# Kernel tuning notes

Hardware: AMD Instinct MI355X
Metric: run time of the kernel (lower is better)

The kernel has to match this reference:

```python
import jax, jax.numpy as jnp
import numpy as np

BASE_THETA = 0.5
K_DOP = 0.2
K_NOR = 0.15
K_SERO = 0.1
DIM = 1024


def setup_inputs() -> dict:
    key = jax.random.key(0)
    ks = jax.random.split(key, 9)
    scale = 1.0 / np.sqrt(DIM)
    x = jax.random.normal(ks[0], (2, 2048, DIM), dtype=jnp.float32)
    Wq = jax.random.normal(ks[1], (DIM, DIM), dtype=jnp.float32) * scale
    bq = jnp.zeros((DIM,), dtype=jnp.float32)
    Wk = jax.random.normal(ks[2], (DIM, DIM), dtype=jnp.float32) * scale
    bk = jnp.zeros((DIM,), dtype=jnp.float32)
    Wv = jax.random.normal(ks[3], (DIM, DIM), dtype=jnp.float32) * scale
    bv = jnp.zeros((DIM,), dtype=jnp.float32)
    Wo = jax.random.normal(ks[4], (DIM, DIM), dtype=jnp.float32) * scale
    bo = jnp.zeros((DIM,), dtype=jnp.float32)
    return {"x": x, "Wq": Wq, "bq": bq, "Wk": Wk, "bk": bk,
            "Wv": Wv, "bv": bv, "Wo": Wo, "bo": bo}


def reference(x, Wq, bq, Wk, bk, Wv, bv, Wo, bo):
    # Projections: torch nn.Linear computes x @ W.T + b
    q = jnp.einsum('bsd,ed->bse', x, Wq) + bq
    k = jnp.einsum('bsd,ed->bse', x, Wk) + bk
    v = jnp.einsum('bsd,ed->bse', x, Wv) + bv
    # Full [B, S, S] scores (no 1/sqrt(d) scaling in the original)
    qk = jnp.einsum('bsd,btd->bst', q, k)
    theta = (BASE_THETA
             + K_DOP * jax.nn.sigmoid(qk)
             + K_NOR * jnp.tanh(qk)
             + K_SERO * jax.nn.relu(qk))
    attn = jax.nn.softmax(theta, axis=-1)
    out = jnp.einsum('bst,btd->bsd', attn, v)
    return jnp.einsum('bsd,ed->bse', out, Wo) + bo
```

## Files before the change

kernel.cpp:

```cpp
#include <hip/hip_runtime.h>
#include <hip/hip_fp16.h>
#include <stdint.h>

typedef _Float16 f16;
typedef __attribute__((ext_vector_type(8))) _Float16 f16x8;
typedef __attribute__((ext_vector_type(4))) _Float16 f16x4;
typedef __attribute__((ext_vector_type(4))) float f32x4;

#define SEQ 2048
#define DIM 1024
#define NBATCH 2
#define MTOT 4096

__global__ void fill_kernel(float* p, float v, int n){
  int i = blockIdx.x * 256 + threadIdx.x;
  if (i < n) p[i] = v;
}

__global__ void cvt_all(const float* __restrict__ x, const float* __restrict__ Wq,
                        const float* __restrict__ Wk, const float* __restrict__ Wv,
                        const float* __restrict__ Wo,
                        f16* __restrict__ x16, f16* __restrict__ Wcat, f16* __restrict__ Wo16,
                        float* __restrict__ rowacc){
  int b = blockIdx.x;
  if (b == 8192){
    float4 z = {0.f, 0.f, 0.f, 0.f};
#pragma unroll
    for (int i = 0; i < 4; i++) ((float4*)rowacc)[threadIdx.x + i * 256] = z;
    return;
  }
  const float* src; f16* dst; int i;
  if (b < 4096){
    src = x; dst = x16; i = b * 256 + threadIdx.x;
  } else {
    int t = (b - 4096) >> 10;
    i = ((b - 4096) & 1023) * 256 + threadIdx.x;
    src = t == 0 ? Wq : t == 1 ? Wk : t == 2 ? Wv : Wo;
    dst = (t == 3) ? Wo16 : Wcat + (size_t)t * DIM * DIM;
  }
  float4 v = ((const float4*)src)[i];
  ((f16x4*)dst)[i] = (f16x4){(f16)v.x, (f16)v.y, (f16)v.z, (f16)v.w};
}

#define GLOAD16(SRC, DST) __builtin_amdgcn_global_load_lds( \
    (__attribute__((address_space(1))) void*)(SRC), \
    (__attribute__((address_space(3))) void*)(DST), 16, 0, 0)

template<int MODE>
__global__ __launch_bounds__(256, 2)
void gemm_k64(const f16* __restrict__ A, const f16* __restrict__ B,
              int K, int lda, int ldb, long bsA, long bsB, long bsC,
              float* __restrict__ Cf, f16* __restrict__ Ch, f16* __restrict__ vT,
              const float* __restrict__ bias0, const float* __restrict__ bias1,
              const float* __restrict__ bias2, float* __restrict__ rowacc,
              int ldc)
{
  __shared__ __align__(16) f16 As[8192];
  __shared__ __align__(16) f16 Bs[8192];
  const int tid  = threadIdx.x;
  const int lane = tid & 63;
  const int wid  = tid >> 6;
  const int bm = blockIdx.x, bn = blockIdx.y, bz = blockIdx.z;

  const int s_r  = tid >> 3;
  const int s_cb = (tid & 7) ^ (s_r & 7);
  const f16* Abase = A + (long)bz * bsA + (long)(bm * 128 + s_r) * lda + s_cb * 8;
  const f16* Bbase = B + (long)bz * bsB + (long)(bn * 128 + s_r) * ldb + s_cb * 8;

#define STG(T) do{ \
    GLOAD16(Abase + (long)(T)*64,                  &As[       tid*8]); \
    GLOAD16(Abase + (long)(T)*64 + (long)32 * lda, &As[2048 + tid*8]); \
    GLOAD16(Abase + (long)(T)*64 + (long)64 * lda, &As[4096 + tid*8]); \
    GLOAD16(Abase + (long)(T)*64 + (long)96 * lda, &As[6144 + tid*8]); \
    GLOAD16(Bbase + (long)(T)*64,                  &Bs[       tid*8]); \
    GLOAD16(Bbase + (long)(T)*64 + (long)32 * ldb, &Bs[2048 + tid*8]); \
    GLOAD16(Bbase + (long)(T)*64 + (long)64 * ldb, &Bs[4096 + tid*8]); \
    GLOAD16(Bbase + (long)(T)*64 + (long)96 * ldb, &Bs[6144 + tid*8]); \
  }while(0)

  const int l15 = lane & 15, l7 = lane & 7, lhi = lane >> 4;
  const int wrow = (wid >> 1) * 64;
  const int wcol = (wid & 1) * 64;
  const int ar = (wrow + l15) * 64;
  const int br = (wcol + l15) * 64;
  const int cb0 = ((0 + lhi) ^ l7) * 8;
  const int cb1 = ((4 + lhi) ^ l7) * 8;

  f32x4 acc[4][4] = {};
  const int NT = K >> 6;

  for (int t = 0; t < NT; ++t){
    __syncthreads();
    STG(t);
    __syncthreads();
    f16x8 af[4], bf[4];
#pragma unroll
    for (int i = 0; i < 4; i++) af[i] = *(const f16x8*)&As[ar + i * 1024 + cb0];
#pragma unroll
    for (int j = 0; j < 4; j++) bf[j] = *(const f16x8*)&Bs[br + j * 1024 + cb0];
#pragma unroll
    for (int i = 0; i < 4; i++)
#pragma unroll
      for (int j = 0; j < 4; j++)
        acc[i][j] = __builtin_amdgcn_mfma_f32_16x16x32_f16(af[i], bf[j], acc[i][j], 0, 0, 0);
#pragma unroll
    for (int i = 0; i < 4; i++) af[i] = *(const f16x8*)&As[ar + i * 1024 + cb1];
#pragma unroll
    for (int j = 0; j < 4; j++) bf[j] = *(const f16x8*)&Bs[br + j * 1024 + cb1];
#pragma unroll
    for (int i = 0; i < 4; i++)
#pragma unroll
      for (int j = 0; j < 4; j++)
        acc[i][j] = __builtin_amdgcn_mfma_f32_16x16x32_f16(af[i], bf[j], acc[i][j], 0, 0, 0);
  }
#undef STG

  const int cc = l15;
  const int rr = lhi * 4;

  if constexpr (MODE == 0){
#pragma unroll
    for (int i = 0; i < 4; i++)
#pragma unroll
      for (int j = 0; j < 4; j++){
        const int col = bn * 128 + wcol + j * 16 + cc;
        const float badd = bias0 ? bias0[col] : 0.f;
#pragma unroll
        for (int r = 0; r < 4; r++){
          const int row = bm * 128 + wrow + i * 16 + rr + r;
          Cf[(long)bz * bsC + (long)row * ldc + col] = acc[i][j][r] + badd;
        }
      }
  } else if constexpr (MODE == 2){
#pragma unroll
    for (int i = 0; i < 4; i++)
#pragma unroll
      for (int r = 0; r < 4; r++){
        const int row = bm * 128 + wrow + i * 16 + rr + r;
        const float inv = 1.f / rowacc[bz * SEQ + row];
#pragma unroll
        for (int j = 0; j < 4; j++){
          const int col = bn * 128 + wcol + j * 16 + cc;
          Ch[(long)bz * bsC + (long)row * ldc + col] = (f16)(acc[i][j][r] * inv);
        }
      }
  } else if constexpr (MODE == 4){
#pragma unroll
    for (int i = 0; i < 4; i++)
#pragma unroll
      for (int j = 0; j < 4; j++){
        const int col = bn * 128 + wcol + j * 16 + cc;
        if (col < 2048){
          const float badd = (col < 1024) ? bias0[col] : bias1[col - 1024];
#pragma unroll
          for (int r = 0; r < 4; r++){
            const int row = bm * 128 + wrow + i * 16 + rr + r;
            Ch[(long)row * ldc + col] = (f16)(acc[i][j][r] + badd);
          }
        } else {
          const int d = col - 2048;
          const float badd = bias2[d];
          const int row0 = bm * 128 + wrow + i * 16 + rr;
          const int b2 = row0 >> 11, t0 = row0 & 2047;
          f16x4 pk = {(f16)(acc[i][j][0] + badd), (f16)(acc[i][j][1] + badd),
                      (f16)(acc[i][j][2] + badd), (f16)(acc[i][j][3] + badd)};
          *(f16x4*)&vT[(long)b2 * DIM * SEQ + (long)d * SEQ + t0] = pk;
        }
      }
  } else {
#pragma unroll
    for (int i = 0; i < 4; i++)
#pragma unroll
      for (int r = 0; r < 4; r++){
        const int row = bm * 128 + wrow + i * 16 + rr + r;
        float rs = 0.f;
#pragma unroll
        for (int j = 0; j < 4; j++){
          const int col = bn * 128 + wcol + j * 16 + cc;
          const float v = acc[i][j][r];
          const float e1 = __expf(-v);
          const float sg = 1.f / (1.f + e1);
          const float e2 = e1 * e1;
          const float th = 2.f / (1.f + e2) - 1.f;
          const float theta = 0.5f + 0.2f * sg + 0.15f * th + 0.1f * fmaxf(v, 0.f);
          const float P = __expf(fminf(theta - 10.f, 11.f));
          Ch[(long)bz * bsC + (long)row * ldc + col] = (f16)P;
          rs += P;
        }
        rs += __shfl_xor(rs, 1, 64);
        rs += __shfl_xor(rs, 2, 64);
        rs += __shfl_xor(rs, 4, 64);
        rs += __shfl_xor(rs, 8, 64);
        if (cc == 0) atomicAdd(&rowacc[bz * SEQ + row], rs);
      }
  }
}

extern "C" void kernel_launch(void* const* d_in, const int* in_sizes, int n_in,
                              void* d_out, int out_size, void* d_ws, size_t ws_size,
                              hipStream_t stream){
  const float* x  = (const float*)d_in[0];
  const float* Wq = (const float*)d_in[1];
  const float* bq = (const float*)d_in[2];
  const float* Wk = (const float*)d_in[3];
  const float* bk = (const float*)d_in[4];
  const float* Wv = (const float*)d_in[5];
  const float* bv = (const float*)d_in[6];
  const float* Wo = (const float*)d_in[7];
  const float* bo = (const float*)d_in[8];
  float* out = (float*)d_out;

  char* ws = (char*)d_ws;
  size_t off = 0;
  auto alloc = [&](size_t bytes) -> char* {
    char* p = ws + off; off += (bytes + 255) & ~(size_t)255; return p;
  };

  f16* x16     = (f16*)alloc(2ull * MTOT * DIM);
  f16* Wcat    = (f16*)alloc(2ull * 3 * DIM * DIM);
  f16* Wo16    = (f16*)alloc(2ull * DIM * DIM);
  f16* qkcat   = (f16*)alloc(2ull * MTOT * 2 * DIM);
  f16* vT      = (f16*)alloc(2ull * NBATCH * DIM * SEQ);
  f16* Pbuf    = (f16*)alloc(2ull * NBATCH * SEQ * SEQ);
  f16* outb    = (f16*)alloc(2ull * MTOT * DIM);
  float* rowac = (float*)alloc(4ull * MTOT);

  if (off > ws_size){
    fill_kernel<<<(out_size + 255) / 256, 256, 0, stream>>>(out, 12345.0f, out_size);
    return;
  }

  cvt_all<<<8193, 256, 0, stream>>>(x, Wq, Wk, Wv, Wo, x16, Wcat, Wo16, rowac);

  gemm_k64<4><<<dim3(MTOT / 128, 3 * DIM / 128, 1), 256, 0, stream>>>(
      x16, Wcat, DIM, DIM, DIM, 0, 0, 0,
      nullptr, qkcat, vT, bq, bk, bv, nullptr, 2 * DIM);

  gemm_k64<5><<<dim3(SEQ / 128, SEQ / 128, NBATCH), 256, 0, stream>>>(
      qkcat, qkcat + DIM, DIM, 2 * DIM, 2 * DIM,
      (long)SEQ * 2 * DIM, (long)SEQ * 2 * DIM, (long)SEQ * SEQ,
      nullptr, Pbuf, nullptr, nullptr, nullptr, nullptr, rowac, SEQ);

  gemm_k64<2><<<dim3(SEQ / 128, DIM / 128, NBATCH), 256, 0, stream>>>(
      Pbuf, vT, SEQ, SEQ, SEQ,
      (long)SEQ * SEQ, (long)DIM * SEQ, (long)SEQ * DIM,
      nullptr, outb, nullptr, nullptr, nullptr, nullptr, rowac, DIM);

  gemm_k64<0><<<dim3(MTOT / 128, DIM / 128, 1), 256, 0, stream>>>(
      outb, Wo16, DIM, DIM, DIM, 0, 0, 0,
      out, nullptr, nullptr, bo, nullptr, nullptr, nullptr, DIM);
}
```

Baseline: 139.2 us.

## Reassociate output projection into V and triple-buffer GEMM LDS pipeline

Computes V·Wo^T before attention, so P·(V Wo^T) plus normalization and bias produces the output directly and the separate output-projection pass over the attention result is dropped. The new V·Wo GEMM writes its result transposed for the PV GEMM. All GEMMs also switch from a K=64 single-buffer loop with two barriers per step to a K=32 three-stage LDS ring that uses async global-to-LDS loads, vmcnt waits and one barrier per step, with occupancy raised to 3 blocks per CU. The reassociation keeps the FLOP count the same, since the extra GEMM matches the one removed. The main gain is expected from overlapping loads with compute, at the cost of more rounding because V Wo is stored as f16.

Result: slower. 146.8 us (+5.5%).

```diff
diff --git a/kernel.cpp b/kernel.cpp
--- a/kernel.cpp
+++ b/kernel.cpp
@@ -47,102 +47,92 @@
     (__attribute__((address_space(3))) void*)(DST), 16, 0, 0)
 
 template<int MODE>
-__global__ __launch_bounds__(256, 2)
-void gemm_k64(const f16* __restrict__ A, const f16* __restrict__ B,
-              int K, int lda, int ldb, long bsA, long bsB, long bsC,
-              float* __restrict__ Cf, f16* __restrict__ Ch, f16* __restrict__ vT,
-              const float* __restrict__ bias0, const float* __restrict__ bias1,
-              const float* __restrict__ bias2, float* __restrict__ rowacc,
-              int ldc)
+__global__ __launch_bounds__(256, 3)
+void gemm_p3(const f16* __restrict__ A, const f16* __restrict__ B,
+             int K, int lda, int ldb, long bsA, long bsB, long bsC,
+             float* __restrict__ Cf, f16* __restrict__ Ch, f16* __restrict__ Ct,
+             const float* __restrict__ bias0, const float* __restrict__ bias1,
+             const float* __restrict__ bias2, float* __restrict__ rowacc,
+             int ldc)
 {
-  __shared__ __align__(16) f16 As[8192];
-  __shared__ __align__(16) f16 Bs[8192];
+  __shared__ __align__(16) f16 As[3][4096];
+  __shared__ __align__(16) f16 Bs[3][4096];
   const int tid  = threadIdx.x;
   const int lane = tid & 63;
   const int wid  = tid >> 6;
   const int bm = blockIdx.x, bn = blockIdx.y, bz = blockIdx.z;
 
-  const int s_r  = tid >> 3;
-  const int s_cb = (tid & 7) ^ (s_r & 7);
-  const f16* Abase = A + (long)bz * bsA + (long)(bm * 128 + s_r) * lda + s_cb * 8;
-  const f16* Bbase = B + (long)bz * bsB + (long)(bn * 128 + s_r) * ldb + s_cb * 8;
-
-#define STG(T) do{ \
-    GLOAD16(Abase + (long)(T)*64,                  &As[       tid*8]); \
-    GLOAD16(Abase + (long)(T)*64 + (long)32 * lda, &As[2048 + tid*8]); \
-    GLOAD16(Abase + (long)(T)*64 + (long)64 * lda, &As[4096 + tid*8]); \
-    GLOAD16(Abase + (long)(T)*64 + (long)96 * lda, &As[6144 + tid*8]); \
-    GLOAD16(Bbase + (long)(T)*64,                  &Bs[       tid*8]); \
-    GLOAD16(Bbase + (long)(T)*64 + (long)32 * ldb, &Bs[2048 + tid*8]); \
-    GLOAD16(Bbase + (long)(T)*64 + (long)64 * ldb, &Bs[4096 + tid*8]); \
-    GLOAD16(Bbase + (long)(T)*64 + (long)96 * ldb, &Bs[6144 + tid*8]); \
+  long aoff[2], boff[2];
+#pragma unroll
+  for (int l = 0; l < 2; l++){
+    const int r64 = (l * 256 + tid) >> 3;
+    const int cb  = (tid & 7) ^ (r64 & 7);
+    const int grow = r64 + 64 * (cb >> 2);
+    const int gk   = (cb & 3) * 8;
+    aoff[l] = (long)(bm * 128 + grow) * lda + gk;
+    boff[l] = (long)(bn * 128 + grow) * ldb + gk;
+  }
+  const f16* Ag = A + (long)bz * bsA;
+  const f16* Bg = B + (long)bz * bsB;
+
+#define STG(E, T) do{ \
+    GLOAD16(Ag + aoff[0] + (long)(T)*32, &As[E][       tid*8]); \
+    GLOAD16(Ag + aoff[1] + (long)(T)*32, &As[E][2048 + tid*8]); \
+    GLOAD16(Bg + boff[0] + (long)(T)*32, &Bs[E][       tid*8]); \
+    GLOAD16(Bg + boff[1] + (long)(T)*32, &Bs[E][2048 + tid*8]); \
   }while(0)
 
-  const int l15 = lane & 15, l7 = lane & 7, lhi = lane >> 4;
+  const int l15 = lane & 15, lhi = lane >> 4;
   const int wrow = (wid >> 1) * 64;
   const int wcol = (wid & 1) * 64;
-  const int ar = (wrow + l15) * 64;
-  const int br = (wcol + l15) * 64;
-  const int cb0 = ((0 + lhi) ^ l7) * 8;
-  const int cb1 = ((4 + lhi) ^ l7) * 8;
+  const int rga = wrow >> 6, rgb = wcol >> 6;
+  int aadr[4], badr[4];
+#pragma unroll
+  for (int i = 0; i < 4; i++){
+    aadr[i] = (i * 16 + l15) * 64 + (((rga * 4 + lhi) ^ (l15 & 7)) * 8);
+    badr[i] = (i * 16 + l15) * 64 + (((rgb * 4 + lhi) ^ (l15 & 7)) * 8);
+  }
 
   f32x4 acc[4][4] = {};
-  const int NT = K >> 6;
+  const int NT = K >> 5;
+
+  STG(0, 0);
+  STG(1, 1);
+  int d = 0, e = 2;
 
   for (int t = 0; t < NT; ++t){
-    __syncthreads();
-    STG(t);
-    __syncthreads();
+    if (t + 1 < NT) asm volatile("s_waitcnt vmcnt(4)" ::: "memory");
+    else            asm volatile("s_waitcnt vmcnt(0)" ::: "memory");
+    __builtin_amdgcn_s_barrier();
+    if (t + 2 < NT) STG(e, t + 2);
     f16x8 af[4], bf[4];
 #pragma unroll
-    for (int i = 0; i < 4; i++) af[i] = *(const f16x8*)&As[ar + i * 1024 + cb0];
-#pragma unroll
-    for (int j = 0; j < 4; j++) bf[j] = *(const f16x8*)&Bs[br + j * 1024 + cb0];
+    for (int i = 0; i < 4; i++) af[i] = *(const f16x8*)&As[d][aadr[i]];
+#pragma unroll
+    for (int j = 0; j < 4; j++) bf[j] = *(const f16x8*)&Bs[d][badr[j]];
 #pragma unroll
     for (int i = 0; i < 4; i++)
 #pragma unroll
       for (int j = 0; j < 4; j++)
         acc[i][j] = __builtin_amdgcn_mfma_f32_16x16x32_f16(af[i], bf[j], acc[i][j], 0, 0, 0);
-#pragma unroll
-    for (int i = 0; i < 4; i++) af[i] = *(const f16x8*)&As[ar + i * 1024 + cb1];
-#pragma unroll
-    for (int j = 0; j < 4; j++) bf[j] = *(const f16x8*)&Bs[br + j * 1024 + cb1];
-#pragma unroll
-    for (int i = 0; i < 4; i++)
-#pragma unroll
-      for (int j = 0; j < 4; j++)
-        acc[i][j] = __builtin_amdgcn_mfma_f32_16x16x32_f16(af[i], bf[j], acc[i][j], 0, 0, 0);
+    d = (d == 2) ? 0 : d + 1;
+    e = (e == 2) ? 0 : e + 1;
   }
 #undef STG
 
   const int cc = l15;
   const int rr = lhi * 4;
 
-  if constexpr (MODE == 0){
+  if constexpr (MODE == 3){
 #pragma unroll
     for (int i = 0; i < 4; i++)
 #pragma unroll
       for (int j = 0; j < 4; j++){
         const int col = bn * 128 + wcol + j * 16 + cc;
-        const float badd = bias0 ? bias0[col] : 0.f;
-#pragma unroll
-        for (int r = 0; r < 4; r++){
-          const int row = bm * 128 + wrow + i * 16 + rr + r;
-          Cf[(long)bz * bsC + (long)row * ldc + col] = acc[i][j][r] + badd;
-        }
-      }
-  } else if constexpr (MODE == 2){
-#pragma unroll
-    for (int i = 0; i < 4; i++)
-#pragma unroll
-      for (int r = 0; r < 4; r++){
-        const int row = bm * 128 + wrow + i * 16 + rr + r;
-        const float inv = 1.f / rowacc[bz * SEQ + row];
-#pragma unroll
-        for (int j = 0; j < 4; j++){
-          const int col = bn * 128 + wcol + j * 16 + cc;
-          Ch[(long)bz * bsC + (long)row * ldc + col] = (f16)(acc[i][j][r] * inv);
-        }
+        const int row0 = bm * 128 + wrow + i * 16 + rr;
+        f16x4 pk = {(f16)acc[i][j][0], (f16)acc[i][j][1],
+                    (f16)acc[i][j][2], (f16)acc[i][j][3]};
+        *(f16x4*)&Ct[(long)bz * DIM * SEQ + (long)col * SEQ + row0] = pk;
       }
   } else if constexpr (MODE == 4){
 #pragma unroll
@@ -158,16 +148,16 @@
             Ch[(long)row * ldc + col] = (f16)(acc[i][j][r] + badd);
           }
         } else {
-          const int d = col - 2048;
-          const float badd = bias2[d];
-          const int row0 = bm * 128 + wrow + i * 16 + rr;
-          const int b2 = row0 >> 11, t0 = row0 & 2047;
-          f16x4 pk = {(f16)(acc[i][j][0] + badd), (f16)(acc[i][j][1] + badd),
-                      (f16)(acc[i][j][2] + badd), (f16)(acc[i][j][3] + badd)};
-          *(f16x4*)&vT[(long)b2 * DIM * SEQ + (long)d * SEQ + t0] = pk;
+          const int dcol = col - 2048;
+          const float badd = bias2[dcol];
+#pragma unroll
+          for (int r = 0; r < 4; r++){
+            const int row = bm * 128 + wrow + i * 16 + rr + r;
+            Ct[(long)row * DIM + dcol] = (f16)(acc[i][j][r] + badd);
+          }
         }
       }
-  } else {
+  } else if constexpr (MODE == 5){
 #pragma unroll
     for (int i = 0; i < 4; i++)
 #pragma unroll
@@ -193,6 +183,19 @@
         rs += __shfl_xor(rs, 8, 64);
         if (cc == 0) atomicAdd(&rowacc[bz * SEQ + row], rs);
       }
+  } else {
+#pragma unroll
+    for (int i = 0; i < 4; i++)
+#pragma unroll
+      for (int r = 0; r < 4; r++){
+        const int row = bm * 128 + wrow + i * 16 + rr + r;
+        const float inv = 1.f / rowacc[bz * SEQ + row];
+#pragma unroll
+        for (int j = 0; j < 4; j++){
+          const int col = bn * 128 + wcol + j * 16 + cc;
+          Cf[(long)bz * bsC + (long)row * ldc + col] = acc[i][j][r] * inv + bias0[col];
+        }
+      }
   }
 }
 
@@ -220,9 +223,9 @@
   f16* Wcat    = (f16*)alloc(2ull * 3 * DIM * DIM);
   f16* Wo16    = (f16*)alloc(2ull * DIM * DIM);
   f16* qkcat   = (f16*)alloc(2ull * MTOT * 2 * DIM);
-  f16* vT      = (f16*)alloc(2ull * NBATCH * DIM * SEQ);
+  f16* vbuf    = (f16*)alloc(2ull * MTOT * DIM);
   f16* Pbuf    = (f16*)alloc(2ull * NBATCH * SEQ * SEQ);
-  f16* outb    = (f16*)alloc(2ull * MTOT * DIM);
+  f16* vWoT    = (f16*)alloc(2ull * NBATCH * DIM * SEQ);
   float* rowac = (float*)alloc(4ull * MTOT);
 
   if (off > ws_size){
@@ -232,21 +235,22 @@
 
   cvt_all<<<8193, 256, 0, stream>>>(x, Wq, Wk, Wv, Wo, x16, Wcat, Wo16, rowac);
 
-  gemm_k64<4><<<dim3(MTOT / 128, 3 * DIM / 128, 1), 256, 0, stream>>>(
+  gemm_p3<4><<<dim3(MTOT / 128, 3 * DIM / 128, 1), 256, 0, stream>>>(
       x16, Wcat, DIM, DIM, DIM, 0, 0, 0,
-      nullptr, qkcat, vT, bq, bk, bv, nullptr, 2 * DIM);
-
-  gemm_k64<5><<<dim3(SEQ / 128, SEQ / 128, NBATCH), 256, 0, stream>>>(
+      nullptr, qkcat, vbuf, bq, bk, bv, nullptr, 2 * DIM);
+
+  gemm_p3<5><<<dim3(SEQ / 128, SEQ / 128, NBATCH), 256, 0, stream>>>(
       qkcat, qkcat + DIM, DIM, 2 * DIM, 2 * DIM,
       (long)SEQ * 2 * DIM, (long)SEQ * 2 * DIM, (long)SEQ * SEQ,
       nullptr, Pbuf, nullptr, nullptr, nullptr, nullptr, rowac, SEQ);
 
-  gemm_k64<2><<<dim3(SEQ / 128, DIM / 128, NBATCH), 256, 0, stream>>>(
-      Pbuf, vT, SEQ, SEQ, SEQ,
+  gemm_p3<3><<<dim3(SEQ / 128, DIM / 128, NBATCH), 256, 0, stream>>>(
+      vbuf, Wo16, DIM, DIM, DIM,
+      (long)SEQ * DIM, 0, 0,
+      nullptr, nullptr, vWoT, nullptr, nullptr, nullptr, nullptr, 0);
+
+  gemm_p3<6><<<dim3(SEQ / 128, DIM / 128, NBATCH), 256, 0, stream>>>(
+      Pbuf, vWoT, SEQ, SEQ, SEQ,
       (long)SEQ * SEQ, (long)DIM * SEQ, (long)SEQ * DIM,
-      nullptr, outb, nullptr, nullptr, nullptr, nullptr, rowac, DIM);
-
-  gemm_k64<0><<<dim3(MTOT / 128, DIM / 128, 1), 256, 0, stream>>>(
-      outb, Wo16, DIM, DIM, DIM, 0, 0, 0,
-      out, nullptr, nullptr, bo, nullptr, nullptr, nullptr, DIM);
-}
+      out, nullptr, nullptr, bo, nullptr, nullptr, rowac, DIM);
+}
```

## Reassociate output projection into V·Woᵀ and merge it with the QK GEMM

Applied to the files above, without the earlier changes.

Uses associativity, attn·(V·Woᵀ) instead of (attn·V)·Woᵀ. The V·Woᵀ product runs in the same launch as the QK-score GEMM through a combined 768-block grid. This removes one dependent GEMM launch and the intermediate out buffer, and the final P·(VWo) GEMM now applies the row normalisation and output bias directly in fp32. The final GEMM uses 512-thread blocks with a narrower per-wave tile, and launch bounds change to 3 blocks per CU. The risk is extra fp16 rounding of V·Woᵀ before the attention sum, and uneven work between the two block kinds in the merged grid.

Measured after the change: 119.5 us. 14.2% less time.

```diff
diff --git a/kernel.cpp b/kernel.cpp
--- a/kernel.cpp
+++ b/kernel.cpp
@@ -46,14 +46,164 @@
     (__attribute__((address_space(1))) void*)(SRC), \
     (__attribute__((address_space(3))) void*)(DST), 16, 0, 0)
 
+__device__ __forceinline__ float theta_exp(float v){
+  const float e1 = __expf(-v);
+  const float sg = 1.f / (1.f + e1);
+  const float e2 = e1 * e1;
+  const float th = 2.f / (1.f + e2) - 1.f;
+  const float theta = 0.5f + 0.2f * sg + 0.15f * th + 0.1f * fmaxf(v, 0.f);
+  return __expf(fminf(theta - 10.f, 11.f));
+}
+
 template<int MODE>
-__global__ __launch_bounds__(256, 2)
-void gemm_k64(const f16* __restrict__ A, const f16* __restrict__ B,
-              int K, int lda, int ldb, long bsA, long bsB, long bsC,
-              float* __restrict__ Cf, f16* __restrict__ Ch, f16* __restrict__ vT,
-              const float* __restrict__ bias0, const float* __restrict__ bias1,
-              const float* __restrict__ bias2, float* __restrict__ rowacc,
-              int ldc)
+__global__ __launch_bounds__(256, 3)
+void gemm256(const f16* __restrict__ A0, const f16* __restrict__ A1,
+             const f16* __restrict__ B0,
+             f16* __restrict__ O0, f16* __restrict__ O1,
+             const float* __restrict__ c0, const float* __restrict__ c1,
+             const float* __restrict__ c2, float* __restrict__ rowacc)
+{
+  __shared__ __align__(16) f16 As[8192];
+  __shared__ __align__(16) f16 Bs[8192];
+  const int tid  = threadIdx.x;
+  const int lane = tid & 63;
+  const int wid  = tid >> 6;
+
+  int bm, bn, bz = 0, lda, ldb;
+  const f16 *Ag, *Bg;
+  bool isQK = true;
+  if constexpr (MODE == 4){
+    bm = blockIdx.x; bn = blockIdx.y; lda = DIM; ldb = DIM;
+    Ag = A0; Bg = B0;
+  } else {
+    const int r = blockIdx.x;
+    if (r < 512){
+      bz = r >> 8; const int q = r & 255; bm = q & 15; bn = q >> 4;
+      Ag = A0 + (long)bz * SEQ * 2048;
+      Bg = A0 + DIM + (long)bz * SEQ * 2048;
+      lda = 2048; ldb = 2048;
+    } else {
+      isQK = false;
+      int q = r - 512; bz = q >> 7; q &= 127; bm = q & 15; bn = q >> 4;
+      Ag = A1 + (long)bz * SEQ * DIM;
+      Bg = B0;
+      lda = DIM; ldb = DIM;
+    }
+  }
+
+  const int s_r  = tid >> 3;
+  const int s_cb = (tid & 7) ^ (s_r & 7);
+  const f16* Ab = Ag + (long)(bm * 128 + s_r) * lda + s_cb * 8;
+  const f16* Bb = Bg + (long)(bn * 128 + s_r) * ldb + s_cb * 8;
+
+  const int l15 = lane & 15, l7 = lane & 7, lhi = lane >> 4;
+  const int wrow = (wid >> 1) * 64;
+  const int wcol = (wid & 1) * 64;
+  const int ar = (wrow + l15) * 64;
+  const int br = (wcol + l15) * 64;
+  const int cb0 = ((0 + lhi) ^ l7) * 8;
+  const int cb1 = ((4 + lhi) ^ l7) * 8;
+
+  f32x4 acc[4][4] = {};
+
+  for (int t = 0; t < 16; ++t){
+    __syncthreads();
+    GLOAD16(Ab + (long)t*64,                  &As[       tid*8]);
+    GLOAD16(Ab + (long)t*64 + (long)32 * lda, &As[2048 + tid*8]);
+    GLOAD16(Ab + (long)t*64 + (long)64 * lda, &As[4096 + tid*8]);
+    GLOAD16(Ab + (long)t*64 + (long)96 * lda, &As[6144 + tid*8]);
+    GLOAD16(Bb + (long)t*64,                  &Bs[       tid*8]);
+    GLOAD16(Bb + (long)t*64 + (long)32 * ldb, &Bs[2048 + tid*8]);
+    GLOAD16(Bb + (long)t*64 + (long)64 * ldb, &Bs[4096 + tid*8]);
+    GLOAD16(Bb + (long)t*64 + (long)96 * ldb, &Bs[6144 + tid*8]);
+    __syncthreads();
+    f16x8 af[4], bf[4];
+#pragma unroll
+    for (int i = 0; i < 4; i++) af[i] = *(const f16x8*)&As[ar + i * 1024 + cb0];
+#pragma unroll
+    for (int j = 0; j < 4; j++) bf[j] = *(const f16x8*)&Bs[br + j * 1024 + cb0];
+#pragma unroll
+    for (int i = 0; i < 4; i++)
+#pragma unroll
+      for (int j = 0; j < 4; j++)
+        acc[i][j] = __builtin_amdgcn_mfma_f32_16x16x32_f16(af[i], bf[j], acc[i][j], 0, 0, 0);
+#pragma unroll
+    for (int i = 0; i < 4; i++) af[i] = *(const f16x8*)&As[ar + i * 1024 + cb1];
+#pragma unroll
+    for (int j = 0; j < 4; j++) bf[j] = *(const f16x8*)&Bs[br + j * 1024 + cb1];
+#pragma unroll
+    for (int i = 0; i < 4; i++)
+#pragma unroll
+      for (int j = 0; j < 4; j++)
+        acc[i][j] = __builtin_amdgcn_mfma_f32_16x16x32_f16(af[i], bf[j], acc[i][j], 0, 0, 0);
+  }
+
+  const int cc = l15;
+  const int rr = lhi * 4;
+
+  if constexpr (MODE == 4){
+#pragma unroll
+    for (int i = 0; i < 4; i++)
+#pragma unroll
+      for (int j = 0; j < 4; j++){
+        const int col = bn * 128 + wcol + j * 16 + cc;
+        if (col < 2048){
+          const float badd = (col < 1024) ? c0[col] : c1[col - 1024];
+#pragma unroll
+          for (int r = 0; r < 4; r++){
+            const int row = bm * 128 + wrow + i * 16 + rr + r;
+            O0[(long)row * 2048 + col] = (f16)(acc[i][j][r] + badd);
+          }
+        } else {
+          const int dcol = col - 2048;
+          const float badd = c2[dcol];
+#pragma unroll
+          for (int r = 0; r < 4; r++){
+            const int row = bm * 128 + wrow + i * 16 + rr + r;
+            O1[(long)row * DIM + dcol] = (f16)(acc[i][j][r] + badd);
+          }
+        }
+      }
+  } else {
+    if (isQK){
+#pragma unroll
+      for (int i = 0; i < 4; i++)
+#pragma unroll
+        for (int r = 0; r < 4; r++){
+          const int row = bm * 128 + wrow + i * 16 + rr + r;
+          float rs = 0.f;
+#pragma unroll
+          for (int j = 0; j < 4; j++){
+            const int col = bn * 128 + wcol + j * 16 + cc;
+            const float P = theta_exp(acc[i][j][r]);
+            O0[(long)bz * SEQ * SEQ + (long)row * SEQ + col] = (f16)P;
+            rs += P;
+          }
+          rs += __shfl_xor(rs, 1, 64);
+          rs += __shfl_xor(rs, 2, 64);
+          rs += __shfl_xor(rs, 4, 64);
+          rs += __shfl_xor(rs, 8, 64);
+          if (cc == 0) atomicAdd(&rowacc[bz * SEQ + row], rs);
+        }
+    } else {
+#pragma unroll
+      for (int i = 0; i < 4; i++)
+#pragma unroll
+        for (int j = 0; j < 4; j++){
+          const int col = bn * 128 + wcol + j * 16 + cc;
+          const int row0 = bm * 128 + wrow + i * 16 + rr;
+          f16x4 pk = {(f16)acc[i][j][0], (f16)acc[i][j][1],
+                      (f16)acc[i][j][2], (f16)acc[i][j][3]};
+          *(f16x4*)&O1[(long)bz * DIM * SEQ + (long)col * SEQ + row0] = pk;
+        }
+    }
+  }
+}
+
+__global__ __launch_bounds__(512, 2)
+void gemm512_final(const f16* __restrict__ Pb, const f16* __restrict__ Vw,
+                   float* __restrict__ out, const float* __restrict__ bo,
+                   const float* __restrict__ rowacc)
 {
   __shared__ __align__(16) f16 As[8192];
   __shared__ __align__(16) f16 Bs[8192];
@@ -62,138 +212,66 @@
   const int wid  = tid >> 6;
   const int bm = blockIdx.x, bn = blockIdx.y, bz = blockIdx.z;
 
+  const f16* Ag = Pb + (long)bz * SEQ * SEQ;
+  const f16* Bg = Vw + (long)bz * DIM * SEQ;
+
   const int s_r  = tid >> 3;
   const int s_cb = (tid & 7) ^ (s_r & 7);
-  const f16* Abase = A + (long)bz * bsA + (long)(bm * 128 + s_r) * lda + s_cb * 8;
-  const f16* Bbase = B + (long)bz * bsB + (long)(bn * 128 + s_r) * ldb + s_cb * 8;
-
-#define STG(T) do{ \
-    GLOAD16(Abase + (long)(T)*64,                  &As[       tid*8]); \
-    GLOAD16(Abase + (long)(T)*64 + (long)32 * lda, &As[2048 + tid*8]); \
-    GLOAD16(Abase + (long)(T)*64 + (long)64 * lda, &As[4096 + tid*8]); \
-    GLOAD16(Abase + (long)(T)*64 + (long)96 * lda, &As[6144 + tid*8]); \
-    GLOAD16(Bbase + (long)(T)*64,                  &Bs[       tid*8]); \
-    GLOAD16(Bbase + (long)(T)*64 + (long)32 * ldb, &Bs[2048 + tid*8]); \
-    GLOAD16(Bbase + (long)(T)*64 + (long)64 * ldb, &Bs[4096 + tid*8]); \
-    GLOAD16(Bbase + (long)(T)*64 + (long)96 * ldb, &Bs[6144 + tid*8]); \
-  }while(0)
+  const f16* Ab = Ag + (long)(bm * 128 + s_r) * SEQ + s_cb * 8;
+  const f16* Bb = Bg + (long)(bn * 128 + s_r) * SEQ + s_cb * 8;
 
   const int l15 = lane & 15, l7 = lane & 7, lhi = lane >> 4;
-  const int wrow = (wid >> 1) * 64;
-  const int wcol = (wid & 1) * 64;
+  const int wrow = (wid >> 2) * 64;
+  const int wcol = (wid & 3) * 32;
   const int ar = (wrow + l15) * 64;
   const int br = (wcol + l15) * 64;
   const int cb0 = ((0 + lhi) ^ l7) * 8;
   const int cb1 = ((4 + lhi) ^ l7) * 8;
 
-  f32x4 acc[4][4] = {};
-  const int NT = K >> 6;
-
-  for (int t = 0; t < NT; ++t){
+  f32x4 acc[4][2] = {};
+
+  for (int t = 0; t < 32; ++t){
     __syncthreads();
-    STG(t);
+    GLOAD16(Ab + (long)t*64,                  &As[       tid*8]);
+    GLOAD16(Ab + (long)t*64 + (long)64 * SEQ, &As[4096 + tid*8]);
+    GLOAD16(Bb + (long)t*64,                  &Bs[       tid*8]);
+    GLOAD16(Bb + (long)t*64 + (long)64 * SEQ, &Bs[4096 + tid*8]);
     __syncthreads();
-    f16x8 af[4], bf[4];
+    f16x8 af[4], bf[2];
 #pragma unroll
     for (int i = 0; i < 4; i++) af[i] = *(const f16x8*)&As[ar + i * 1024 + cb0];
 #pragma unroll
-    for (int j = 0; j < 4; j++) bf[j] = *(const f16x8*)&Bs[br + j * 1024 + cb0];
-#pragma unroll
-    for (int i = 0; i < 4; i++)
-#pragma unroll
-      for (int j = 0; j < 4; j++)
+    for (int j = 0; j < 2; j++) bf[j] = *(const f16x8*)&Bs[br + j * 1024 + cb0];
+#pragma unroll
+    for (int i = 0; i < 4; i++)
+#pragma unroll
+      for (int j = 0; j < 2; j++)
         acc[i][j] = __builtin_amdgcn_mfma_f32_16x16x32_f16(af[i], bf[j], acc[i][j], 0, 0, 0);
 #pragma unroll
     for (int i = 0; i < 4; i++) af[i] = *(const f16x8*)&As[ar + i * 1024 + cb1];
 #pragma unroll
-    for (int j = 0; j < 4; j++) bf[j] = *(const f16x8*)&Bs[br + j * 1024 + cb1];
-#pragma unroll
-    for (int i = 0; i < 4; i++)
-#pragma unroll
-      for (int j = 0; j < 4; j++)
+    for (int j = 0; j < 2; j++) bf[j] = *(const f16x8*)&Bs[br + j * 1024 + cb1];
+#pragma unroll
+    for (int i = 0; i < 4; i++)
+#pragma unroll
+      for (int j = 0; j < 2; j++)
         acc[i][j] = __builtin_amdgcn_mfma_f32_16x16x32_f16(af[i], bf[j], acc[i][j], 0, 0, 0);
   }
-#undef STG
 
   const int cc = l15;
   const int rr = lhi * 4;
-
-  if constexpr (MODE == 0){
-#pragma unroll
-    for (int i = 0; i < 4; i++)
-#pragma unroll
-      for (int j = 0; j < 4; j++){
+#pragma unroll
+  for (int i = 0; i < 4; i++)
+#pragma unroll
+    for (int r = 0; r < 4; r++){
+      const int row = bm * 128 + wrow + i * 16 + rr + r;
+      const float inv = 1.f / rowacc[bz * SEQ + row];
+#pragma unroll
+      for (int j = 0; j < 2; j++){
         const int col = bn * 128 + wcol + j * 16 + cc;
-        const float badd = bias0 ? bias0[col] : 0.f;
-#pragma unroll
-        for (int r = 0; r < 4; r++){
-          const int row = bm * 128 + wrow + i * 16 + rr + r;
-          Cf[(long)bz * bsC + (long)row * ldc + col] = acc[i][j][r] + badd;
-        }
+        out[(long)bz * SEQ * DIM + (long)row * DIM + col] = acc[i][j][r] * inv + bo[col];
       }
-  } else if constexpr (MODE == 2){
-#pragma unroll
-    for (int i = 0; i < 4; i++)
-#pragma unroll
-      for (int r = 0; r < 4; r++){
-        const int row = bm * 128 + wrow + i * 16 + rr + r;
-        const float inv = 1.f / rowacc[bz * SEQ + row];
-#pragma unroll
-        for (int j = 0; j < 4; j++){
-          const int col = bn * 128 + wcol + j * 16 + cc;
-          Ch[(long)bz * bsC + (long)row * ldc + col] = (f16)(acc[i][j][r] * inv);
-        }
-      }
-  } else if constexpr (MODE == 4){
-#pragma unroll
-    for (int i = 0; i < 4; i++)
-#pragma unroll
-      for (int j = 0; j < 4; j++){
-        const int col = bn * 128 + wcol + j * 16 + cc;
-        if (col < 2048){
-          const float badd = (col < 1024) ? bias0[col] : bias1[col - 1024];
-#pragma unroll
-          for (int r = 0; r < 4; r++){
-            const int row = bm * 128 + wrow + i * 16 + rr + r;
-            Ch[(long)row * ldc + col] = (f16)(acc[i][j][r] + badd);
-          }
-        } else {
-          const int d = col - 2048;
-          const float badd = bias2[d];
-          const int row0 = bm * 128 + wrow + i * 16 + rr;
-          const int b2 = row0 >> 11, t0 = row0 & 2047;
-          f16x4 pk = {(f16)(acc[i][j][0] + badd), (f16)(acc[i][j][1] + badd),
-                      (f16)(acc[i][j][2] + badd), (f16)(acc[i][j][3] + badd)};
-          *(f16x4*)&vT[(long)b2 * DIM * SEQ + (long)d * SEQ + t0] = pk;
-        }
-      }
-  } else {
-#pragma unroll
-    for (int i = 0; i < 4; i++)
-#pragma unroll
-      for (int r = 0; r < 4; r++){
-        const int row = bm * 128 + wrow + i * 16 + rr + r;
-        float rs = 0.f;
-#pragma unroll
-        for (int j = 0; j < 4; j++){
-          const int col = bn * 128 + wcol + j * 16 + cc;
-          const float v = acc[i][j][r];
-          const float e1 = __expf(-v);
-          const float sg = 1.f / (1.f + e1);
-          const float e2 = e1 * e1;
-          const float th = 2.f / (1.f + e2) - 1.f;
-          const float theta = 0.5f + 0.2f * sg + 0.15f * th + 0.1f * fmaxf(v, 0.f);
-          const float P = __expf(fminf(theta - 10.f, 11.f));
-          Ch[(long)bz * bsC + (long)row * ldc + col] = (f16)P;
-          rs += P;
-        }
-        rs += __shfl_xor(rs, 1, 64);
-        rs += __shfl_xor(rs, 2, 64);
-        rs += __shfl_xor(rs, 4, 64);
-        rs += __shfl_xor(rs, 8, 64);
-        if (cc == 0) atomicAdd(&rowacc[bz * SEQ + row], rs);
-      }
-  }
+    }
 }
 
 extern "C" void kernel_launch(void* const* d_in, const int* in_sizes, int n_in,
@@ -220,9 +298,9 @@
   f16* Wcat    = (f16*)alloc(2ull * 3 * DIM * DIM);
   f16* Wo16    = (f16*)alloc(2ull * DIM * DIM);
   f16* qkcat   = (f16*)alloc(2ull * MTOT * 2 * DIM);
-  f16* vT      = (f16*)alloc(2ull * NBATCH * DIM * SEQ);
+  f16* vbuf    = (f16*)alloc(2ull * MTOT * DIM);
   f16* Pbuf    = (f16*)alloc(2ull * NBATCH * SEQ * SEQ);
-  f16* outb    = (f16*)alloc(2ull * MTOT * DIM);
+  f16* vWoT    = (f16*)alloc(2ull * NBATCH * DIM * SEQ);
   float* rowac = (float*)alloc(4ull * MTOT);
 
   if (off > ws_size){
@@ -232,21 +310,12 @@
 
   cvt_all<<<8193, 256, 0, stream>>>(x, Wq, Wk, Wv, Wo, x16, Wcat, Wo16, rowac);
 
-  gemm_k64<4><<<dim3(MTOT / 128, 3 * DIM / 128, 1), 256, 0, stream>>>(
-      x16, Wcat, DIM, DIM, DIM, 0, 0, 0,
-      nullptr, qkcat, vT, bq, bk, bv, nullptr, 2 * DIM);
-
-  gemm_k64<5><<<dim3(SEQ / 128, SEQ / 128, NBATCH), 256, 0, stream>>>(
-      qkcat, qkcat + DIM, DIM, 2 * DIM, 2 * DIM,
-      (long)SEQ * 2 * DIM, (long)SEQ * 2 * DIM, (long)SEQ * SEQ,
-      nullptr, Pbuf, nullptr, nullptr, nullptr, nullptr, rowac, SEQ);
-
-  gemm_k64<2><<<dim3(SEQ / 128, DIM / 128, NBATCH), 256, 0, stream>>>(
-      Pbuf, vT, SEQ, SEQ, SEQ,
-      (long)SEQ * SEQ, (long)DIM * SEQ, (long)SEQ * DIM,
-      nullptr, outb, nullptr, nullptr, nullptr, nullptr, rowac, DIM);
-
-  gemm_k64<0><<<dim3(MTOT / 128, DIM / 128, 1), 256, 0, stream>>>(
-      outb, Wo16, DIM, DIM, DIM, 0, 0, 0,
-      out, nullptr, nullptr, bo, nullptr, nullptr, nullptr, DIM);
-}
+  gemm256<4><<<dim3(MTOT / 128, 3 * DIM / 128, 1), 256, 0, stream>>>(
+      x16, nullptr, Wcat, qkcat, vbuf, bq, bk, bv, nullptr);
+
+  gemm256<7><<<768, 256, 0, stream>>>(
+      qkcat, vbuf, Wo16, Pbuf, vWoT, nullptr, nullptr, nullptr, rowac);
+
+  gemm512_final<<<dim3(SEQ / 128, DIM / 128, NBATCH), 512, 0, stream>>>(
+      Pbuf, vWoT, out, bo, rowac);
+}
```
